# Optimization experiments

Hardware: AMD Instinct MI355X
Metric: run time of the kernel (lower is better)

The kernel has to match this reference:

```python
import jax, jax.numpy as jnp
import numpy as np


def setup_inputs() -> dict:
    key = jax.random.key(0)
    ks = jax.random.split(key, 6)
    B, T, Din, Dout = 128, 512, 256, 512
    s0 = 1.0 / np.sqrt(Din + Dout)
    s1 = 1.0 / np.sqrt(Dout + Dout)
    return {
        "x": jax.random.normal(ks[0], (B, T, Din), dtype=jnp.float32),
        "W_zr0": jax.random.normal(ks[1], (Din + Dout, 2 * Dout), dtype=jnp.float32) * s0,
        "b_zr0": jnp.zeros((2 * Dout,), dtype=jnp.float32),
        "W_h0": jax.random.normal(ks[2], (Din + Dout, Dout), dtype=jnp.float32) * s0,
        "b_h0": jnp.zeros((Dout,), dtype=jnp.float32),
        "W_zr1": jax.random.normal(ks[3], (Dout + Dout, 2 * Dout), dtype=jnp.float32) * s1,
        "b_zr1": jnp.zeros((2 * Dout,), dtype=jnp.float32),
        "W_h1": jax.random.normal(ks[4], (Dout + Dout, Dout), dtype=jnp.float32) * s1,
        "b_h1": jnp.zeros((Dout,), dtype=jnp.float32),
    }


def _gru_layer(x_seq, W_zr, b_zr, W_h, b_h):
    # x_seq: [B, T, D_in]; returns [B, T, D_out]
    hidden_dim = W_h.shape[1]

    def step(state, xt):
        ins = jnp.concatenate([xt, state], axis=-1)
        zr = jax.nn.sigmoid(ins @ W_zr + b_zr)
        z, r = jnp.split(zr, 2, axis=-1)
        cand_in = jnp.concatenate([xt, z * state], axis=-1)
        h_tmp = jnp.tanh(cand_in @ W_h + b_h)
        h = r * state + (1.0 - r) * h_tmp
        return h, h

    h0 = jnp.zeros((x_seq.shape[0], hidden_dim), dtype=x_seq.dtype)
    _, ys = jax.lax.scan(step, h0, jnp.swapaxes(x_seq, 0, 1))  # scan over time
    return jnp.swapaxes(ys, 0, 1)


def reference(x, W_zr0, b_zr0, W_h0, b_h0, W_zr1, b_zr1, W_h1, b_h1):
    h = _gru_layer(x, W_zr0, b_zr0, W_h0, b_h0)
    h = _gru_layer(h, W_zr1, b_zr1, W_h1, b_h1)
    return h
```

## Files before the change

### kernel.cpp

```cpp
#include <hip/hip_runtime.h>

#define NB 128
#define NT 512
#define DIN 256
#define DD 512

using bf16x8 = __attribute__((ext_vector_type(8))) short;
using f32x4v = __attribute__((ext_vector_type(4))) float;
using u32x4  = __attribute__((ext_vector_type(4))) unsigned int;

__device__ __forceinline__ unsigned short f2bf(float f) {
  unsigned int u = __builtin_bit_cast(unsigned int, f);
  u = (u + 0x7fffu + ((u >> 16) & 1u)) >> 16;
  return (unsigned short)u;
}
__device__ __forceinline__ float bf2f(unsigned short h) {
  unsigned int u = ((unsigned int)h) << 16;
  return __builtin_bit_cast(float, u);
}
__device__ __forceinline__ unsigned int packf(float v) {
  unsigned short hi = f2bf(v);
  unsigned short lo = f2bf(v - bf2f(hi));
  return (((unsigned int)hi) << 16) | lo;
}

__global__ void prep_kernel(const float* __restrict__ x, unsigned int* __restrict__ x_pk,
                            unsigned int* __restrict__ hp, unsigned int* __restrict__ cnt) {
  long i = (long)blockIdx.x * blockDim.x + threadIdx.x;
  const long stride = (long)gridDim.x * blockDim.x;
  const long NX = (long)NB * NT * DIN;
  for (long j = i; j < NX; j += stride) x_pk[j] = packf(x[j]);
  const long NH = 2L * 2 * NB * DD;
  for (long j = i; j < NH; j += stride) hp[j] = 0u;
  if (i < 4096) cnt[i] = 0u;
}

__device__ __forceinline__ void unpack16(const u32x4& q0, const u32x4& q1,
                                         bf16x8& hi, bf16x8& lo) {
  #pragma unroll
  for (int j = 0; j < 4; ++j) {
    hi[j]     = (short)(q0[j] >> 16);
    lo[j]     = (short)(q0[j] & 0xffffu);
    hi[4 + j] = (short)(q1[j] >> 16);
    lo[4 + j] = (short)(q1[j] & 0xffffu);
  }
}

template<int KN>
__device__ __forceinline__ void gemm_pk(const unsigned int* __restrict__ a,
                                        const unsigned short* __restrict__ b,
                                        int quad, f32x4v& cH0, f32x4v& cL0,
                                        f32x4v& cH1, f32x4v& cL1) {
  const unsigned int* ap = a + quad * 8;
  const unsigned short* bp = b + quad * 8;
  #pragma unroll
  for (int kk = 0; kk < KN; kk += 64) {
    u32x4 q0 = *(const u32x4*)(ap + kk);
    u32x4 q1 = *(const u32x4*)(ap + kk + 4);
    u32x4 q2 = *(const u32x4*)(ap + kk + 32);
    u32x4 q3 = *(const u32x4*)(ap + kk + 36);
    bf16x8 a0h, a0l, a1h, a1l;
    unpack16(q0, q1, a0h, a0l);
    unpack16(q2, q3, a1h, a1l);
    bf16x8 b0 = *(const bf16x8*)(bp + kk);
    bf16x8 b1 = *(const bf16x8*)(bp + kk + 32);
    cH0 = __builtin_amdgcn_mfma_f32_16x16x32_bf16(a0h, b0, cH0, 0, 0, 0);
    cL0 = __builtin_amdgcn_mfma_f32_16x16x32_bf16(a0l, b0, cL0, 0, 0, 0);
    cH1 = __builtin_amdgcn_mfma_f32_16x16x32_bf16(a1h, b1, cH1, 0, 0, 0);
    cL1 = __builtin_amdgcn_mfma_f32_16x16x32_bf16(a1l, b1, cL1, 0, 0, 0);
  }
}

template<int KN>
__device__ __forceinline__ void gemm_pk2(const unsigned int* __restrict__ a,
                                         const unsigned short* __restrict__ b0,
                                         const unsigned short* __restrict__ b1,
                                         int quad,
                                         f32x4v& zH0, f32x4v& zL0, f32x4v& zH1, f32x4v& zL1,
                                         f32x4v& rH0, f32x4v& rL0, f32x4v& rH1, f32x4v& rL1) {
  const unsigned int* ap = a + quad * 8;
  const unsigned short* b0p = b0 + quad * 8;
  const unsigned short* b1p = b1 + quad * 8;
  #pragma unroll
  for (int kk = 0; kk < KN; kk += 64) {
    u32x4 q0 = *(const u32x4*)(ap + kk);
    u32x4 q1 = *(const u32x4*)(ap + kk + 4);
    u32x4 q2 = *(const u32x4*)(ap + kk + 32);
    u32x4 q3 = *(const u32x4*)(ap + kk + 36);
    bf16x8 a0h, a0l, a1h, a1l;
    unpack16(q0, q1, a0h, a0l);
    unpack16(q2, q3, a1h, a1l);
    bf16x8 bz0 = *(const bf16x8*)(b0p + kk);
    bf16x8 bz1 = *(const bf16x8*)(b0p + kk + 32);
    bf16x8 br0 = *(const bf16x8*)(b1p + kk);
    bf16x8 br1 = *(const bf16x8*)(b1p + kk + 32);
    zH0 = __builtin_amdgcn_mfma_f32_16x16x32_bf16(a0h, bz0, zH0, 0, 0, 0);
    zL0 = __builtin_amdgcn_mfma_f32_16x16x32_bf16(a0l, bz0, zL0, 0, 0, 0);
    rH0 = __builtin_amdgcn_mfma_f32_16x16x32_bf16(a0h, br0, rH0, 0, 0, 0);
    rL0 = __builtin_amdgcn_mfma_f32_16x16x32_bf16(a0l, br0, rL0, 0, 0, 0);
    zH1 = __builtin_amdgcn_mfma_f32_16x16x32_bf16(a1h, bz1, zH1, 0, 0, 0);
    zL1 = __builtin_amdgcn_mfma_f32_16x16x32_bf16(a1l, bz1, zL1, 0, 0, 0);
    rH1 = __builtin_amdgcn_mfma_f32_16x16x32_bf16(a1h, br1, rH1, 0, 0, 0);
    rL1 = __builtin_amdgcn_mfma_f32_16x16x32_bf16(a1l, br1, rL1, 0, 0, 0);
  }
}

__device__ __forceinline__ void gbarrier(unsigned int* gf, int slot, int w, int lane,
                                         unsigned int rnd) {
  __syncthreads();
  if (threadIdx.x == 0)
    __hip_atomic_store(gf + slot * 16, rnd, __ATOMIC_RELAXED, __HIP_MEMORY_SCOPE_AGENT);
  if (w == 0) {
    for (;;) {
      unsigned int v = __hip_atomic_load(gf + lane * 16, __ATOMIC_RELAXED,
                                         __HIP_MEMORY_SCOPE_AGENT);
      if (__all((int)(v >= rnd))) break;
      __builtin_amdgcn_s_sleep(1);
    }
    if (lane == 0)
      (void)__hip_atomic_load(gf, __ATOMIC_ACQUIRE, __HIP_MEMORY_SCOPE_AGENT);
  }
  __syncthreads();
}

__global__ void __launch_bounds__(512, 1) gru_kernel(
    const float* __restrict__ Wzr0, const float* __restrict__ bzr0,
    const float* __restrict__ Wh0,  const float* __restrict__ bh0,
    const float* __restrict__ Wzr1, const float* __restrict__ bzr1,
    const float* __restrict__ Wh1,  const float* __restrict__ bh1,
    const unsigned int* __restrict__ x_pk, unsigned int* __restrict__ hp,
    unsigned int* __restrict__ zs, unsigned int* __restrict__ cnt,
    float* __restrict__ out)
{
  extern __shared__ __align__(16) unsigned char smem[];
  const int bid = blockIdx.x, tid = threadIdx.x;
  const int w = tid >> 6, lane = tid & 63, quad = lane >> 4, l16 = lane & 15;
  const int l  = bid >> 7;
  const int rb = (bid >> 5) & 3;
  const int cb = bid & 31;
  const int r0 = rb << 5;
  const int c0 = cb << 4;
  const int K  = l ? 1024 : 768;
  const int ldw = K + 8;

  unsigned short* wlds = (unsigned short*)smem;
  float* s_lds = (float*)(smem + ((48 * ldw * 2 + 15) & ~15));
  float* r_lds = s_lds + 512;
  float* pscr  = r_lds + 512;

  const float* Wzr = l ? Wzr1 : Wzr0;
  const float* Wh  = l ? Wh1 : Wh0;
  for (int idx = tid; idx < 16 * K; idx += 512) {
    int j = idx / K, k = idx - j * K;
    wlds[j * ldw + k]        = f2bf(Wzr[k * (2 * DD) + c0 + j]);
    wlds[(16 + j) * ldw + k] = f2bf(Wzr[k * (2 * DD) + DD + c0 + j]);
    wlds[(32 + j) * ldw + k] = f2bf(Wh[k * DD + c0 + j]);
  }
  for (int idx = tid; idx < 512; idx += 512) s_lds[idx] = 0.f;
  const float bz = (l ? bzr1 : bzr0)[c0 + l16];
  const float br = (l ? bzr1 : bzr0)[DD + c0 + l16];
  const float bh = (l ? bh1 : bh0)[c0 + l16];
  __syncthreads();

  unsigned int* gf = cnt + rb * 1024;
  const int slot = l * 32 + cb;
  unsigned int rnd = 0;

  const int rowHalf = w >> 2, seg = w & 3;
  const int gRow = r0 + (rowHalf << 4) + l16;
  const int pidx = (quad << 2) * 16 + l16;

  for (int s = 0; s <= NT; ++s) {
    const int p  = (s + 1) & 1;
    const int pw = s & 1;
    const bool act = l ? (s >= 1) : (s < NT);
    const int t = l ? (s - 1) : s;

    if (act) {
      f32x4v zH0 = {0,0,0,0}, zL0 = {0,0,0,0}, zH1 = {0,0,0,0}, zL1 = {0,0,0,0};
      f32x4v rH0 = {0,0,0,0}, rL0 = {0,0,0,0}, rH1 = {0,0,0,0}, rL1 = {0,0,0,0};
      const unsigned short* bzseg = wlds + l16 * ldw;
      const unsigned short* brseg = wlds + (16 + l16) * ldw;
      if (l == 0) {
        const unsigned int* xa = x_pk + ((long)gRow * NT + t) * DIN;
        const unsigned int* ha = hp + ((p * 2 + 0) * NB + gRow) * DD;
        if      (seg == 0) gemm_pk2<256>(xa, bzseg, brseg, quad,
                                         zH0, zL0, zH1, zL1, rH0, rL0, rH1, rL1);
        else if (seg == 1) gemm_pk2<192>(ha, bzseg + 256, brseg + 256, quad,
                                         zH0, zL0, zH1, zL1, rH0, rL0, rH1, rL1);
        else if (seg == 2) gemm_pk2<192>(ha + 192, bzseg + 448, brseg + 448, quad,
                                         zH0, zL0, zH1, zL1, rH0, rL0, rH1, rL1);
        else               gemm_pk2<128>(ha + 384, bzseg + 640, brseg + 640, quad,
                                         zH0, zL0, zH1, zL1, rH0, rL0, rH1, rL1);
      } else {
        const unsigned int* h0a = hp + ((p * 2 + 0) * NB + gRow) * DD;
        const unsigned int* h1a = hp + ((p * 2 + 1) * NB + gRow) * DD;
        if      (seg == 0) gemm_pk2<256>(h0a, bzseg, brseg, quad,
                                         zH0, zL0, zH1, zL1, rH0, rL0, rH1, rL1);
        else if (seg == 1) gemm_pk2<256>(h0a + 256, bzseg + 256, brseg + 256, quad,
                                         zH0, zL0, zH1, zL1, rH0, rL0, rH1, rL1);
        else if (seg == 2) gemm_pk2<256>(h1a, bzseg + 512, brseg + 512, quad,
                                         zH0, zL0, zH1, zL1, rH0, rL0, rH1, rL1);
        else               gemm_pk2<256>(h1a + 256, bzseg + 768, brseg + 768, quad,
                                         zH0, zL0, zH1, zL1, rH0, rL0, rH1, rL1);
      }
      float zt[4], rt[4];
      #pragma unroll
      for (int i = 0; i < 4; ++i) {
        zt[i] = (zH0[i] + zL0[i]) + (zH1[i] + zL1[i]);
        rt[i] = (rH0[i] + rL0[i]) + (rH1[i] + rL1[i]);
      }
      if (seg) {
        float* pp = pscr + rowHalf * 1536 + (seg - 1) * 512;
        #pragma unroll
        for (int i = 0; i < 4; ++i) {
          pp[pidx + i * 16]       = zt[i];
          pp[256 + pidx + i * 16] = rt[i];
        }
      }
      __syncthreads();
      if (seg == 0) {
        const float* pp = pscr + rowHalf * 1536;
        #pragma unroll
        for (int i = 0; i < 4; ++i) {
          int rloc = (rowHalf << 4) + (quad << 2) + i;
          float zpre = zt[i] + pp[pidx + i * 16] + pp[512 + pidx + i * 16]
                     + pp[1024 + pidx + i * 16] + bz;
          float rpre = rt[i] + pp[256 + pidx + i * 16] + pp[768 + pidx + i * 16]
                     + pp[1280 + pidx + i * 16] + br;
          float zg = 1.f / (1.f + __expf(-zpre));
          float rg = 1.f / (1.f + __expf(-rpre));
          float sv = s_lds[rloc * 16 + l16];
          __hip_atomic_store(&zs[((long)l * NB + r0 + rloc) * DD + c0 + l16],
                             packf(zg * sv), __ATOMIC_RELAXED, __HIP_MEMORY_SCOPE_AGENT);
          r_lds[rloc * 16 + l16] = rg;
        }
      }
    }
    ++rnd;
    gbarrier(gf, slot, w, lane, rnd);

    if (act) {
      f32x4v cH0 = {0,0,0,0}, cL0 = {0,0,0,0}, cH1 = {0,0,0,0}, cL1 = {0,0,0,0};
      const unsigned short* hseg = wlds + (32 + l16) * ldw;
      if (l == 0) {
        const unsigned int* xa = x_pk + ((long)gRow * NT + t) * DIN;
        const unsigned int* za = zs + ((long)l * NB + gRow) * DD;
        if      (seg == 0) gemm_pk<256>(xa, hseg, quad, cH0, cL0, cH1, cL1);
        else if (seg == 1) gemm_pk<192>(za, hseg + 256, quad, cH0, cL0, cH1, cL1);
        else if (seg == 2) gemm_pk<192>(za + 192, hseg + 448, quad, cH0, cL0, cH1, cL1);
        else               gemm_pk<128>(za + 384, hseg + 640, quad, cH0, cL0, cH1, cL1);
      } else {
        const unsigned int* h0a = hp + ((p * 2 + 0) * NB + gRow) * DD;
        const unsigned int* za = zs + ((long)l * NB + gRow) * DD;
        if      (seg == 0) gemm_pk<256>(h0a, hseg, quad, cH0, cL0, cH1, cL1);
        else if (seg == 1) gemm_pk<256>(h0a + 256, hseg + 256, quad, cH0, cL0, cH1, cL1);
        else if (seg == 2) gemm_pk<256>(za, hseg + 512, quad, cH0, cL0, cH1, cL1);
        else               gemm_pk<256>(za + 256, hseg + 768, quad, cH0, cL0, cH1, cL1);
      }
      f32x4v tot;
      #pragma unroll
      for (int i = 0; i < 4; ++i) tot[i] = (cH0[i] + cL0[i]) + (cH1[i] + cL1[i]);
      if (seg) {
        float* pp = pscr + rowHalf * 768 + (seg - 1) * 256;
        #pragma unroll
        for (int i = 0; i < 4; ++i) pp[pidx + i * 16] = tot[i];
      }
      __syncthreads();
      if (seg == 0) {
        const float* pp = pscr + rowHalf * 768;
        #pragma unroll
        for (int i = 0; i < 4; ++i) {
          int rloc = (rowHalf << 4) + (quad << 2) + i;
          float pre = tot[i] + pp[pidx + i * 16] + pp[256 + pidx + i * 16]
                    + pp[512 + pidx + i * 16] + bh;
          float ax = fabsf(pre), e = __expf(-2.f * ax);
          float th = (1.f - e) / (1.f + e);
          th = (pre < 0.f) ? -th : th;
          float rv = r_lds[rloc * 16 + l16];
          float sv = s_lds[rloc * 16 + l16];
          float h = rv * sv + (1.f - rv) * th;
          s_lds[rloc * 16 + l16] = h;
          __hip_atomic_store(&hp[((pw * 2 + l) * NB + r0 + rloc) * DD + c0 + l16],
                             packf(h), __ATOMIC_RELAXED, __HIP_MEMORY_SCOPE_AGENT);
          if (l) out[((long)(r0 + rloc) * NT + t) * DD + c0 + l16] = h;
        }
      }
    }
    ++rnd;
    gbarrier(gf, slot, w, lane, rnd);
  }
}

extern "C" void kernel_launch(void* const* d_in, const int* in_sizes, int n_in,
                              void* d_out, int out_size, void* d_ws, size_t ws_size,
                              hipStream_t stream) {
  const float* x    = (const float*)d_in[0];
  const float* Wzr0 = (const float*)d_in[1];
  const float* bzr0 = (const float*)d_in[2];
  const float* Wh0  = (const float*)d_in[3];
  const float* bh0  = (const float*)d_in[4];
  const float* Wzr1 = (const float*)d_in[5];
  const float* bzr1 = (const float*)d_in[6];
  const float* Wh1  = (const float*)d_in[7];
  const float* bh1  = (const float*)d_in[8];
  float* out = (float*)d_out;

  char* pp = (char*)d_ws;
  unsigned int* cnt  = (unsigned int*)pp;  pp += 16384;
  unsigned int* x_pk = (unsigned int*)pp;  pp += (size_t)NB * NT * DIN * 4;
  unsigned int* hp   = (unsigned int*)pp;  pp += (size_t)2 * 2 * NB * DD * 4;
  unsigned int* zs   = (unsigned int*)pp;  pp += (size_t)2 * NB * DD * 4;

  hipLaunchKernelGGL(prep_kernel, dim3(1024), dim3(256), 0, stream, x, x_pk, hp, cnt);

  const int SMEM = ((48 * (1024 + 8) * 2 + 15) & ~15) + 2 * 512 * 4 + 3072 * 4;
  (void)hipFuncSetAttribute((const void*)gru_kernel,
                            hipFuncAttributeMaxDynamicSharedMemorySize, SMEM);
  hipLaunchKernelGGL(gru_kernel, dim3(256), dim3(512), SMEM, stream,
                     Wzr0, bzr0, Wh0, bh0, Wzr1, bzr1, Wh1, bh1,
                     x_pk, hp, zs, cnt, out);
}
```

Baseline: 6.837 ms.

## Split grid barrier into arrive/wait and keep input operands in registers across phases

The grid barrier is split into an arrive step and a per-wave wait step. Waves whose operands do not depend on other blocks' results (the x-input wave in layer 0, the layer-0 h waves in layer 1) skip the wait and start their GEMM early. Input fragments are loaded once into registers and reused for both the zr and candidate GEMMs instead of being reloaded. The launch-bounds occupancy hint is raised to 2, which may squeeze register allocation given the extra 64 u32x4 prefetch registers, and the per-wave waits add polling traffic.

```diff
diff --git a/kernel.cpp b/kernel.cpp
--- a/kernel.cpp
+++ b/kernel.cpp
@@ -43,6 +43,68 @@
     lo[j]     = (short)(q0[j] & 0xffffu);
     hi[4 + j] = (short)(q1[j] >> 16);
     lo[4 + j] = (short)(q1[j] & 0xffffu);
+  }
+}
+
+template<int KN> struct APF { u32x4 q[KN >> 4]; };
+
+template<int KN>
+__device__ __forceinline__ void apf_load(APF<KN>& r, const unsigned int* __restrict__ a,
+                                         int quad) {
+  const unsigned int* ap = a + quad * 8;
+  #pragma unroll
+  for (int c = 0; c < KN / 64; ++c) {
+    r.q[4 * c + 0] = *(const u32x4*)(ap + 64 * c + 0);
+    r.q[4 * c + 1] = *(const u32x4*)(ap + 64 * c + 4);
+    r.q[4 * c + 2] = *(const u32x4*)(ap + 64 * c + 32);
+    r.q[4 * c + 3] = *(const u32x4*)(ap + 64 * c + 36);
+  }
+}
+
+template<int KN>
+__device__ __forceinline__ void apf_gemm(const APF<KN>& r, const unsigned short* __restrict__ b,
+                                         int quad, f32x4v& cH0, f32x4v& cL0,
+                                         f32x4v& cH1, f32x4v& cL1) {
+  const unsigned short* bp = b + quad * 8;
+  #pragma unroll
+  for (int c = 0; c < KN / 64; ++c) {
+    bf16x8 a0h, a0l, a1h, a1l;
+    unpack16(r.q[4 * c + 0], r.q[4 * c + 1], a0h, a0l);
+    unpack16(r.q[4 * c + 2], r.q[4 * c + 3], a1h, a1l);
+    bf16x8 b0 = *(const bf16x8*)(bp + 64 * c);
+    bf16x8 b1 = *(const bf16x8*)(bp + 64 * c + 32);
+    cH0 = __builtin_amdgcn_mfma_f32_16x16x32_bf16(a0h, b0, cH0, 0, 0, 0);
+    cL0 = __builtin_amdgcn_mfma_f32_16x16x32_bf16(a0l, b0, cL0, 0, 0, 0);
+    cH1 = __builtin_amdgcn_mfma_f32_16x16x32_bf16(a1h, b1, cH1, 0, 0, 0);
+    cL1 = __builtin_amdgcn_mfma_f32_16x16x32_bf16(a1l, b1, cL1, 0, 0, 0);
+  }
+}
+
+template<int KN>
+__device__ __forceinline__ void apf_gemm2(const APF<KN>& r,
+                                          const unsigned short* __restrict__ b0,
+                                          const unsigned short* __restrict__ b1, int quad,
+                                          f32x4v& zH0, f32x4v& zL0, f32x4v& zH1, f32x4v& zL1,
+                                          f32x4v& rH0, f32x4v& rL0, f32x4v& rH1, f32x4v& rL1) {
+  const unsigned short* b0p = b0 + quad * 8;
+  const unsigned short* b1p = b1 + quad * 8;
+  #pragma unroll
+  for (int c = 0; c < KN / 64; ++c) {
+    bf16x8 a0h, a0l, a1h, a1l;
+    unpack16(r.q[4 * c + 0], r.q[4 * c + 1], a0h, a0l);
+    unpack16(r.q[4 * c + 2], r.q[4 * c + 3], a1h, a1l);
+    bf16x8 bz0 = *(const bf16x8*)(b0p + 64 * c);
+    bf16x8 bz1 = *(const bf16x8*)(b0p + 64 * c + 32);
+    bf16x8 br0 = *(const bf16x8*)(b1p + 64 * c);
+    bf16x8 br1 = *(const bf16x8*)(b1p + 64 * c + 32);
+    zH0 = __builtin_amdgcn_mfma_f32_16x16x32_bf16(a0h, bz0, zH0, 0, 0, 0);
+    zL0 = __builtin_amdgcn_mfma_f32_16x16x32_bf16(a0l, bz0, zL0, 0, 0, 0);
+    rH0 = __builtin_amdgcn_mfma_f32_16x16x32_bf16(a0h, br0, rH0, 0, 0, 0);
+    rL0 = __builtin_amdgcn_mfma_f32_16x16x32_bf16(a0l, br0, rL0, 0, 0, 0);
+    zH1 = __builtin_amdgcn_mfma_f32_16x16x32_bf16(a1h, bz1, zH1, 0, 0, 0);
+    zL1 = __builtin_amdgcn_mfma_f32_16x16x32_bf16(a1l, bz1, zL1, 0, 0, 0);
+    rH1 = __builtin_amdgcn_mfma_f32_16x16x32_bf16(a1h, br1, rH1, 0, 0, 0);
+    rL1 = __builtin_amdgcn_mfma_f32_16x16x32_bf16(a1l, br1, rL1, 0, 0, 0);
   }
 }
 
@@ -105,25 +167,23 @@
   }
 }
 
-__device__ __forceinline__ void gbarrier(unsigned int* gf, int slot, int w, int lane,
-                                         unsigned int rnd) {
+__device__ __forceinline__ void garrive(unsigned int* gf, int slot, unsigned int rnd) {
   __syncthreads();
   if (threadIdx.x == 0)
     __hip_atomic_store(gf + slot * 16, rnd, __ATOMIC_RELAXED, __HIP_MEMORY_SCOPE_AGENT);
-  if (w == 0) {
-    for (;;) {
-      unsigned int v = __hip_atomic_load(gf + lane * 16, __ATOMIC_RELAXED,
-                                         __HIP_MEMORY_SCOPE_AGENT);
-      if (__all((int)(v >= rnd))) break;
-      __builtin_amdgcn_s_sleep(1);
-    }
-    if (lane == 0)
-      (void)__hip_atomic_load(gf, __ATOMIC_ACQUIRE, __HIP_MEMORY_SCOPE_AGENT);
-  }
-  __syncthreads();
-}
-
-__global__ void __launch_bounds__(512, 1) gru_kernel(
+}
+__device__ __forceinline__ void gwait(unsigned int* gf, int lane, unsigned int rnd) {
+  for (;;) {
+    unsigned int v = __hip_atomic_load(gf + lane * 16, __ATOMIC_RELAXED,
+                                       __HIP_MEMORY_SCOPE_AGENT);
+    if (__all((int)(v >= rnd))) break;
+    __builtin_amdgcn_s_sleep(1);
+  }
+  if (lane == 0)
+    (void)__hip_atomic_load(gf, __ATOMIC_ACQUIRE, __HIP_MEMORY_SCOPE_AGENT);
+}
+
+__global__ void __launch_bounds__(512, 2) gru_kernel(
     const float* __restrict__ Wzr0, const float* __restrict__ bzr0,
     const float* __restrict__ Wh0,  const float* __restrict__ bh0,
     const float* __restrict__ Wzr1, const float* __restrict__ bzr1,
@@ -169,6 +229,7 @@
   const int rowHalf = w >> 2, seg = w & 3;
   const int gRow = r0 + (rowHalf << 4) + l16;
   const int pidx = (quad << 2) * 16 + l16;
+  const bool isInput = l ? (seg <= 1) : (seg == 0);
 
   for (int s = 0; s <= NT; ++s) {
     const int p  = (s + 1) & 1;
@@ -176,7 +237,10 @@
     const bool act = l ? (s >= 1) : (s < NT);
     const int t = l ? (s - 1) : s;
 
+    APF<256> AIN;
+
     if (act) {
+      if (!(l == 0 && seg == 0)) gwait(gf, lane, rnd);
       f32x4v zH0 = {0,0,0,0}, zL0 = {0,0,0,0}, zH1 = {0,0,0,0}, zL1 = {0,0,0,0};
       f32x4v rH0 = {0,0,0,0}, rL0 = {0,0,0,0}, rH1 = {0,0,0,0}, rL1 = {0,0,0,0};
       const unsigned short* bzseg = wlds + l16 * ldw;
@@ -184,8 +248,10 @@
       if (l == 0) {
         const unsigned int* xa = x_pk + ((long)gRow * NT + t) * DIN;
         const unsigned int* ha = hp + ((p * 2 + 0) * NB + gRow) * DD;
-        if      (seg == 0) gemm_pk2<256>(xa, bzseg, brseg, quad,
-                                         zH0, zL0, zH1, zL1, rH0, rL0, rH1, rL1);
+        if (seg == 0) {
+          apf_load(AIN, xa, quad);
+          apf_gemm2(AIN, bzseg, brseg, quad, zH0, zL0, zH1, zL1, rH0, rL0, rH1, rL1);
+        }
         else if (seg == 1) gemm_pk2<192>(ha, bzseg + 256, brseg + 256, quad,
                                          zH0, zL0, zH1, zL1, rH0, rL0, rH1, rL1);
         else if (seg == 2) gemm_pk2<192>(ha + 192, bzseg + 448, brseg + 448, quad,
@@ -195,10 +261,15 @@
       } else {
         const unsigned int* h0a = hp + ((p * 2 + 0) * NB + gRow) * DD;
         const unsigned int* h1a = hp + ((p * 2 + 1) * NB + gRow) * DD;
-        if      (seg == 0) gemm_pk2<256>(h0a, bzseg, brseg, quad,
-                                         zH0, zL0, zH1, zL1, rH0, rL0, rH1, rL1);
-        else if (seg == 1) gemm_pk2<256>(h0a + 256, bzseg + 256, brseg + 256, quad,
-                                         zH0, zL0, zH1, zL1, rH0, rL0, rH1, rL1);
+        if (seg == 0) {
+          apf_load(AIN, h0a, quad);
+          apf_gemm2(AIN, bzseg, brseg, quad, zH0, zL0, zH1, zL1, rH0, rL0, rH1, rL1);
+        }
+        else if (seg == 1) {
+          apf_load(AIN, h0a + 256, quad);
+          apf_gemm2(AIN, bzseg + 256, brseg + 256, quad,
+                    zH0, zL0, zH1, zL1, rH0, rL0, rH1, rL1);
+        }
         else if (seg == 2) gemm_pk2<256>(h1a, bzseg + 512, brseg + 512, quad,
                                          zH0, zL0, zH1, zL1, rH0, rL0, rH1, rL1);
         else               gemm_pk2<256>(h1a + 256, bzseg + 768, brseg + 768, quad,
@@ -238,23 +309,22 @@
       }
     }
     ++rnd;
-    gbarrier(gf, slot, w, lane, rnd);
+    garrive(gf, slot, rnd);
 
     if (act) {
+      if (!isInput) gwait(gf, lane, rnd);
       f32x4v cH0 = {0,0,0,0}, cL0 = {0,0,0,0}, cH1 = {0,0,0,0}, cL1 = {0,0,0,0};
       const unsigned short* hseg = wlds + (32 + l16) * ldw;
       if (l == 0) {
-        const unsigned int* xa = x_pk + ((long)gRow * NT + t) * DIN;
         const unsigned int* za = zs + ((long)l * NB + gRow) * DD;
-        if      (seg == 0) gemm_pk<256>(xa, hseg, quad, cH0, cL0, cH1, cL1);
+        if      (seg == 0) apf_gemm(AIN, hseg, quad, cH0, cL0, cH1, cL1);
         else if (seg == 1) gemm_pk<192>(za, hseg + 256, quad, cH0, cL0, cH1, cL1);
         else if (seg == 2) gemm_pk<192>(za + 192, hseg + 448, quad, cH0, cL0, cH1, cL1);
         else               gemm_pk<128>(za + 384, hseg + 640, quad, cH0, cL0, cH1, cL1);
       } else {
-        const unsigned int* h0a = hp + ((p * 2 + 0) * NB + gRow) * DD;
         const unsigned int* za = zs + ((long)l * NB + gRow) * DD;
-        if      (seg == 0) gemm_pk<256>(h0a, hseg, quad, cH0, cL0, cH1, cL1);
-        else if (seg == 1) gemm_pk<256>(h0a + 256, hseg + 256, quad, cH0, cL0, cH1, cL1);
+        if      (seg == 0) apf_gemm(AIN, hseg, quad, cH0, cL0, cH1, cL1);
+        else if (seg == 1) apf_gemm(AIN, hseg + 256, quad, cH0, cL0, cH1, cL1);
         else if (seg == 2) gemm_pk<256>(za, hseg + 512, quad, cH0, cL0, cH1, cL1);
         else               gemm_pk<256>(za + 256, hseg + 768, quad, cH0, cL0, cH1, cL1);
       }
@@ -288,7 +358,7 @@
       }
     }
     ++rnd;
-    gbarrier(gf, slot, w, lane, rnd);
+    garrive(gf, slot, rnd);
   }
 }
 
```

New measurement: 15.00 ms. 2.19x slower.
